# Kernel tuning notes

Hardware: AMD Instinct MI355X
Metric: run time of the kernel (lower is better)

Reference implementation:

```python
import jax, jax.numpy as jnp
import numpy as np

ALPHA = 1.702   # GLU sigmoid scale
LIMIT = 7.0     # clamp limit
K = 2           # experts per token


def setup_inputs() -> dict:
    key = jax.random.key(0)
    ks = jax.random.split(key, 4)
    B, S, H, E, I = 1, 1024, 1024, 8, 1024
    return {
        "hidden_states": jax.random.normal(ks[0], (B, S, H), jnp.float32),
        "router_weight": jax.random.normal(ks[1], (E, H), jnp.float32),
        "router_bias": jnp.zeros((E,), jnp.float32),
        "gate_up_proj": jax.random.normal(ks[2], (E, H, 2 * I), jnp.float32) * 0.02,
        "gate_up_bias": jnp.zeros((E, 2 * I), jnp.float32),
        "down_proj": jax.random.normal(ks[3], (E, I, H), jnp.float32) * 0.02,
        "down_bias": jnp.zeros((E, H), jnp.float32),
    }


def reference(hidden_states, router_weight, router_bias, gate_up_proj,
              gate_up_bias, down_proj, down_bias):
    B, S, H = hidden_states.shape
    E = router_weight.shape[0]
    I = down_proj.shape[1]
    T = B * S

    flat = hidden_states.reshape(T, H)

    # Router: softmax over experts, top-K selection (weights NOT renormalized).
    logits = flat @ router_weight.T + router_bias               # [T, E]
    scores = jax.nn.softmax(logits, axis=-1)
    topk_vals, topk_idx = jax.lax.top_k(scores, K)              # [T, K]

    # Dense per-token expert weight matrix (equivalent of dispatch metadata +
    # combine * topk_weights in the tt pipeline); top-k indices are unique.
    w = jnp.zeros((T, E), scores.dtype).at[
        jnp.arange(T)[:, None], topk_idx].set(topk_vals)        # [T, E]

    # Expert MLP with clamped GLU (gpt-oss style).
    gu = jnp.einsum('th,ehf->tef', flat, gate_up_proj) + gate_up_bias  # [T,E,2I]
    gate = jnp.minimum(gu[..., :I], LIMIT)
    up = jnp.clip(gu[..., I:], -LIMIT, LIMIT)
    glu = gate * jax.nn.sigmoid(gate * ALPHA)
    act = (up + 1.0) * glu                                       # [T, E, I]

    down = jnp.einsum('tei,eih->teh', act, down_proj) + down_bias  # [T, E, H]

    # Weighted combine over selected experts.
    out = jnp.einsum('teh,te->th', down, w)
    return out.reshape(B, S, H)
```

## Files before the change

### kernel.cpp

```cpp
#include <hip/hip_runtime.h>
#include <hip/hip_bf16.h>


typedef unsigned short u16;
typedef __attribute__((ext_vector_type(8))) __bf16 bf16x8;
typedef __attribute__((ext_vector_type(4))) float f32x4;

#define T_TOK 1024
#define H_DIM 1024
#define E_NUM 8
#define I_DIM 1024
#define ALPHA 1.702f
#define LIMIT 7.0f
#define LSTR 72

__device__ __forceinline__ u16 f2bf(float f) {
    unsigned u = __builtin_bit_cast(unsigned, f);
    u = (u + 0x7FFFu + ((u >> 16) & 1u)) >> 16;
    return (u16)u;
}

__device__ __forceinline__ unsigned pk2(float lo, float hi) {
#if defined(__has_builtin) && __has_builtin(__builtin_amdgcn_cvt_pk_bf16_f32)
    typedef __attribute__((ext_vector_type(2))) __bf16 bf16x2_t;
    bf16x2_t v = __builtin_amdgcn_cvt_pk_bf16_f32(lo, hi);
    return __builtin_bit_cast(unsigned, v);
#else
    return (unsigned)f2bf(lo) | ((unsigned)f2bf(hi) << 16);
#endif
}

__device__ __forceinline__ f32x4 mfma16(bf16x8 a, bf16x8 b, f32x4 c) {
    return __builtin_amdgcn_mfma_f32_16x16x32_bf16(a, b, c, 0, 0, 0);
}

__device__ __forceinline__ void expert_range(const int* counts, int e,
                                             int& cnt, int& abase) {
    int a = 0, c = 0;
#pragma unroll
    for (int i = 0; i < E_NUM; ++i) {
        int v = counts[i];
        if (i < e) a += v;
        if (i == e) c = v;
    }
    cnt = c; abase = a;
}

__global__ void k_zero(int* counts) {
    if (threadIdx.x < E_NUM) counts[threadIdx.x] = 0;
}

__global__ __launch_bounds__(256) void k_router(
    const float* __restrict__ x, const float* __restrict__ rw,
    const float* __restrict__ rb, const float* __restrict__ db,
    int* __restrict__ counts, int* __restrict__ tok_list,
    float* __restrict__ w_list, u16* __restrict__ xb,
    float* __restrict__ out)
{
    const int t = blockIdx.x;
    const int tid = threadIdx.x;
    const float4 xv = *(const float4*)(x + (size_t)t * H_DIM + tid * 4);

    *(uint2*)(xb + (size_t)t * H_DIM + tid * 4) =
        make_uint2(pk2(xv.x, xv.y), pk2(xv.z, xv.w));

    float p[E_NUM];
#pragma unroll
    for (int e = 0; e < E_NUM; ++e) {
        const float4 wv = *(const float4*)(rw + e * H_DIM + tid * 4);
        p[e] = xv.x * wv.x + xv.y * wv.y + xv.z * wv.z + xv.w * wv.w;
    }
#pragma unroll
    for (int off = 32; off; off >>= 1) {
#pragma unroll
        for (int e = 0; e < E_NUM; ++e) p[e] += __shfl_down(p[e], off, 64);
    }
    __shared__ float red[4][E_NUM];
    __shared__ int se[2];
    __shared__ float sw[2];
    const int lane = tid & 63, wvid = tid >> 6;
    if (lane == 0) {
#pragma unroll
        for (int e = 0; e < E_NUM; ++e) red[wvid][e] = p[e];
    }
    __syncthreads();
    if (tid == 0) {
        float lg[E_NUM];
#pragma unroll
        for (int e = 0; e < E_NUM; ++e)
            lg[e] = red[0][e] + red[1][e] + red[2][e] + red[3][e] + rb[e];
        float m1 = -1e30f, m2 = -1e30f; int i1 = 0, i2 = 0;
#pragma unroll
        for (int e = 0; e < E_NUM; ++e) {
            float l = lg[e];
            if (l > m1) { m2 = m1; i2 = i1; m1 = l; i1 = e; }
            else if (l > m2) { m2 = l; i2 = e; }
        }
        float s = 0.f;
#pragma unroll
        for (int e = 0; e < E_NUM; ++e) s += __expf(lg[e] - m1);
        const float w0 = 1.0f / s;
        const float w1 = __expf(m2 - m1) / s;
        int slot0 = atomicAdd(&counts[i1], 1);
        tok_list[i1 * T_TOK + slot0] = t;
        w_list[i1 * T_TOK + slot0] = w0;
        int slot1 = atomicAdd(&counts[i2], 1);
        tok_list[i2 * T_TOK + slot1] = t;
        w_list[i2 * T_TOK + slot1] = w1;
        se[0] = i1; se[1] = i2; sw[0] = w0; sw[1] = w1;
    }
    __syncthreads();
    const int e0 = se[0], e1 = se[1];
    const float w0 = sw[0], w1 = sw[1];
    const int c = tid * 4;
    float4 d0 = *(const float4*)(db + e0 * H_DIM + c);
    float4 d1 = *(const float4*)(db + e1 * H_DIM + c);
    float4 o;
    o.x = w0 * d0.x + w1 * d1.x;
    o.y = w0 * d0.y + w1 * d1.y;
    o.z = w0 * d0.z + w1 * d1.z;
    o.w = w0 * d0.w + w1 * d1.w;
    *(float4*)(out + (size_t)t * H_DIM + c) = o;
}

__global__ __launch_bounds__(256, 4) void k_gateup(
    const float* __restrict__ gup, const float* __restrict__ gub,
    const int* __restrict__ counts, const int* __restrict__ tok_list,
    const u16* __restrict__ xb, u16* __restrict__ act)
{
    const int e = blockIdx.z;
    int cnt, abase;
    expert_range(counts, e, cnt, abase);
    const int m0 = blockIdx.y * 64;
    if (m0 >= cnt) return;
    const int n0 = blockIdx.x * 32;
    const int tid = threadIdx.x;

    __shared__ __align__(16) u16 As0[64 * LSTR];
    __shared__ __align__(16) u16 Bs0[64 * LSTR];
    __shared__ __align__(16) u16 As1[64 * LSTR];
    __shared__ __align__(16) u16 Bs1[64 * LSTR];
    unsigned* B32_0 = (unsigned*)Bs0;
    unsigned* B32_1 = (unsigned*)Bs1;

    const int arow_i = tid >> 2, akq = (tid & 3) * 16;
    const int aslot = m0 + arow_i;
    const int atok = (aslot < cnt) ? tok_list[e * T_TOK + aslot] : 0;
    const u16* asrc = xb + (size_t)atok * H_DIM + akq;
    u16* adst0 = &As0[arow_i * LSTR + akq];
    u16* adst1 = &As1[arow_i * LSTR + akq];

    const int kp = tid >> 3, q = tid & 7;
    const float* bgate = gup + ((size_t)e << 21) + n0 + q * 4;

    const int lane = tid & 63, wv = tid >> 6;
    const int fm = lane & 15, kg = lane >> 4;

    f32x4 accg[2], accu[2];
#pragma unroll
    for (int nt = 0; nt < 2; ++nt) {
        accg[nt] = (f32x4){0.f, 0.f, 0.f, 0.f};
        accu[nt] = (f32x4){0.f, 0.f, 0.f, 0.f};
    }

#define GU_LOAD(A0, A1, G0, G1, U0, U1, KB)                                    \
    {                                                                          \
        const u16* ap_ = asrc + (KB);                                          \
        A0 = *(const uint4*)(ap_);                                             \
        A1 = *(const uint4*)(ap_ + 8);                                         \
        const float* gp_ = bgate + (size_t)((KB) + 2 * kp) * 2048;             \
        G0 = *(const float4*)(gp_);                                            \
        G1 = *(const float4*)(gp_ + 2048);                                     \
        U0 = *(const float4*)(gp_ + 1024);                                     \
        U1 = *(const float4*)(gp_ + 3072);                                     \
    }
#define GU_STORE(AD, B32, A0, A1, G0, G1, U0, U1)                              \
    {                                                                          \
        *(uint4*)(AD)       = A0;                                              \
        *(uint4*)((AD) + 8) = A1;                                              \
        const float* g0_ = (const float*)&G0; const float* g1_ = (const float*)&G1; \
        const float* u0_ = (const float*)&U0; const float* u1_ = (const float*)&U1; \
        _Pragma("unroll")                                                      \
        for (int j = 0; j < 4; ++j) {                                          \
            B32[(q * 4 + j) * 36 + kp]        = pk2(g0_[j], g1_[j]);           \
            B32[(32 + q * 4 + j) * 36 + kp]   = pk2(u0_[j], u1_[j]);           \
        }                                                                      \
    }
#define GU_MFMA(AS, BS)                                                        \
    {                                                                          \
        _Pragma("unroll")                                                      \
        for (int sub = 0; sub < 2; ++sub) {                                    \
            bf16x8 af = *(const bf16x8*)&AS[(wv * 16 + fm) * LSTR + sub * 32 + kg * 8]; \
            _Pragma("unroll")                                                  \
            for (int nt = 0; nt < 2; ++nt) {                                   \
                bf16x8 bg = *(const bf16x8*)&BS[(nt * 16 + fm) * LSTR + sub * 32 + kg * 8]; \
                bf16x8 bu = *(const bf16x8*)&BS[(32 + nt * 16 + fm) * LSTR + sub * 32 + kg * 8]; \
                accg[nt] = mfma16(af, bg, accg[nt]);                           \
                accu[nt] = mfma16(af, bu, accu[nt]);                           \
            }                                                                  \
        }                                                                      \
    }

    uint4 a0s0, a1s0, a0s1, a1s1;
    float4 g0s0, g1s0, u0s0, u1s0, g0s1, g1s1, u0s1, u1s1;
    GU_LOAD(a0s0, a1s0, g0s0, g1s0, u0s0, u1s0, 0);
    GU_LOAD(a0s1, a1s1, g0s1, g1s1, u0s1, u1s1, 64);
    GU_STORE(adst0, B32_0, a0s0, a1s0, g0s0, g1s0, u0s0, u1s0);
    GU_LOAD(a0s0, a1s0, g0s0, g1s0, u0s0, u1s0, 128);
    __syncthreads();

    for (int kb = 0; kb < H_DIM; kb += 128) {
        GU_STORE(adst1, B32_1, a0s1, a1s1, g0s1, g1s1, u0s1, u1s1);
        if (kb + 192 < H_DIM)
            GU_LOAD(a0s1, a1s1, g0s1, g1s1, u0s1, u1s1, kb + 192);
        GU_MFMA(As0, Bs0);
        __syncthreads();
        if (kb + 128 < H_DIM) {
            GU_STORE(adst0, B32_0, a0s0, a1s0, g0s0, g1s0, u0s0, u1s0);
            if (kb + 256 < H_DIM)
                GU_LOAD(a0s0, a1s0, g0s0, g1s0, u0s0, u1s0, kb + 256);
        }
        GU_MFMA(As1, Bs1);
        __syncthreads();
    }
#undef GU_LOAD
#undef GU_STORE
#undef GU_MFMA

#pragma unroll
    for (int r = 0; r < 4; ++r) {
        int rowb = wv * 16 + kg * 4 + r;
        int slot = m0 + rowb;
        if (slot >= cnt) continue;
        size_t arow_o = (size_t)(abase + slot) * I_DIM;
#pragma unroll
        for (int nt = 0; nt < 2; ++nt) {
            int cn = n0 + nt * 16 + fm;
            float g = accg[nt][r] + gub[e * 2048 + cn];
            float u = accu[nt][r] + gub[e * 2048 + 1024 + cn];
            g = fminf(g, LIMIT);
            u = fminf(fmaxf(u, -LIMIT), LIMIT);
            float glu = g / (1.f + __expf(-ALPHA * g));
            act[arow_o + cn] = f2bf((u + 1.f) * glu);
        }
    }
}

__global__ __launch_bounds__(256, 4) void k_down(
    const float* __restrict__ dp,
    const int* __restrict__ counts, const int* __restrict__ tok_list,
    const float* __restrict__ w_list,
    const u16* __restrict__ act, float* __restrict__ out)
{
    const int e = blockIdx.z & 7, ks = blockIdx.z >> 3;
    int cnt, abase;
    expert_range(counts, e, cnt, abase);
    const int m0 = blockIdx.y * 64;
    if (m0 >= cnt) return;
    const int n0 = blockIdx.x * 64;
    const int tid = threadIdx.x;

    __shared__ __align__(16) u16 As0[64 * LSTR];
    __shared__ __align__(16) u16 Bs0[64 * LSTR];
    __shared__ __align__(16) u16 As1[64 * LSTR];
    __shared__ __align__(16) u16 Bs1[64 * LSTR];
    unsigned* B32_0 = (unsigned*)Bs0;
    unsigned* B32_1 = (unsigned*)Bs1;

    const int arow_i = tid >> 2, akq = (tid & 3) * 16;
    const u16* asrc = act + (size_t)(abase + m0 + arow_i) * I_DIM + ks * 512 + akq;
    u16* adst0 = &As0[arow_i * LSTR + akq];
    u16* adst1 = &As1[arow_i * LSTR + akq];

    const int kp = tid >> 3, q = tid & 7;
    const float* bsrc = dp + ((size_t)e << 20) + (size_t)(ks * 512) * 1024 + n0 + q * 4;

    const int lane = tid & 63, wv = tid >> 6;
    const int fm = lane & 15, kg = lane >> 4;

    f32x4 acc[4];
#pragma unroll
    for (int nt = 0; nt < 4; ++nt) acc[nt] = (f32x4){0.f, 0.f, 0.f, 0.f};

#define DN_LOAD(A0, A1, B00, B01, B10, B11, KB)                                \
    {                                                                          \
        const u16* ap_ = asrc + (KB);                                          \
        A0 = *(const uint4*)(ap_);                                             \
        A1 = *(const uint4*)(ap_ + 8);                                         \
        const float* bp_ = bsrc + (size_t)((KB) + 2 * kp) * 1024;              \
        B00 = *(const float4*)(bp_);                                           \
        B01 = *(const float4*)(bp_ + 1024);                                    \
        B10 = *(const float4*)(bp_ + 32);                                      \
        B11 = *(const float4*)(bp_ + 1056);                                    \
    }
#define DN_STORE(AD, B32, A0, A1, B00, B01, B10, B11)                          \
    {                                                                          \
        *(uint4*)(AD)       = A0;                                              \
        *(uint4*)((AD) + 8) = A1;                                              \
        const float* b00_ = (const float*)&B00; const float* b01_ = (const float*)&B01; \
        const float* b10_ = (const float*)&B10; const float* b11_ = (const float*)&B11; \
        _Pragma("unroll")                                                      \
        for (int j = 0; j < 4; ++j) {                                          \
            B32[(q * 4 + j) * 36 + kp]      = pk2(b00_[j], b01_[j]);           \
            B32[(32 + q * 4 + j) * 36 + kp] = pk2(b10_[j], b11_[j]);           \
        }                                                                      \
    }
#define DN_MFMA(AS, BS)                                                        \
    {                                                                          \
        _Pragma("unroll")                                                      \
        for (int sub = 0; sub < 2; ++sub) {                                    \
            bf16x8 af = *(const bf16x8*)&AS[(wv * 16 + fm) * LSTR + sub * 32 + kg * 8]; \
            _Pragma("unroll")                                                  \
            for (int nt = 0; nt < 4; ++nt) {                                   \
                bf16x8 b = *(const bf16x8*)&BS[(nt * 16 + fm) * LSTR + sub * 32 + kg * 8]; \
                acc[nt] = mfma16(af, b, acc[nt]);                              \
            }                                                                  \
        }                                                                      \
    }

    uint4 a0s0, a1s0, a0s1, a1s1;
    float4 b00s0, b01s0, b10s0, b11s0, b00s1, b01s1, b10s1, b11s1;
    DN_LOAD(a0s0, a1s0, b00s0, b01s0, b10s0, b11s0, 0);
    DN_LOAD(a0s1, a1s1, b00s1, b01s1, b10s1, b11s1, 64);
    DN_STORE(adst0, B32_0, a0s0, a1s0, b00s0, b01s0, b10s0, b11s0);
    DN_LOAD(a0s0, a1s0, b00s0, b01s0, b10s0, b11s0, 128);
    __syncthreads();

    for (int kb = 0; kb < 512; kb += 128) {
        DN_STORE(adst1, B32_1, a0s1, a1s1, b00s1, b01s1, b10s1, b11s1);
        if (kb + 192 < 512)
            DN_LOAD(a0s1, a1s1, b00s1, b01s1, b10s1, b11s1, kb + 192);
        DN_MFMA(As0, Bs0);
        __syncthreads();
        if (kb + 128 < 512) {
            DN_STORE(adst0, B32_0, a0s0, a1s0, b00s0, b01s0, b10s0, b11s0);
            if (kb + 256 < 512)
                DN_LOAD(a0s0, a1s0, b00s0, b01s0, b10s0, b11s0, kb + 256);
        }
        DN_MFMA(As1, Bs1);
        __syncthreads();
    }
#undef DN_LOAD
#undef DN_STORE
#undef DN_MFMA

#pragma unroll
    for (int r = 0; r < 4; ++r) {
        int rowb = wv * 16 + kg * 4 + r;
        int slot = m0 + rowb;
        if (slot >= cnt) continue;
        float wgt = w_list[e * T_TOK + slot];
        int tok = tok_list[e * T_TOK + slot];
        float* orow = out + (size_t)tok * H_DIM + n0;
#pragma unroll
        for (int nt = 0; nt < 4; ++nt)
            atomicAdd(orow + nt * 16 + fm, acc[nt][r] * wgt);
    }
}

extern "C" void kernel_launch(void* const* d_in, const int* in_sizes, int n_in,
                              void* d_out, int out_size, void* d_ws, size_t ws_size,
                              hipStream_t stream) {
    const float* x   = (const float*)d_in[0];
    const float* rw  = (const float*)d_in[1];
    const float* rb  = (const float*)d_in[2];
    const float* gup = (const float*)d_in[3];
    const float* gub = (const float*)d_in[4];
    const float* dp  = (const float*)d_in[5];
    const float* db  = (const float*)d_in[6];
    float* out = (float*)d_out;

    char* ws = (char*)d_ws;
    int*   counts   = (int*)(ws);
    int*   tok_list = (int*)(ws + 64);
    float* w_list   = (float*)(ws + 64 + 32768);
    u16*   xb       = (u16*)(ws + 65600);
    u16*   act      = (u16*)(ws + 65600 + 2097152);

    k_zero<<<1, 64, 0, stream>>>(counts);
    k_router<<<T_TOK, 256, 0, stream>>>(x, rw, rb, db, counts, tok_list, w_list,
                                        xb, out);
    k_gateup<<<dim3(32, 16, 8), 256, 0, stream>>>(gup, gub, counts, tok_list,
                                                  xb, act);
    k_down<<<dim3(16, 16, 16), 256, 0, stream>>>(dp, counts, tok_list, w_list,
                                                 act, out);
}
```

Baseline: 213.8 us.

## Pre-convert expert weights to transposed bf16 and stage tiles via global_load_lds

Adds a conversion kernel that turns gate_up and down weights into transposed bf16 buffers in workspace on every call. The GEMM kernels then load A and B tiles straight into LDS with global_load_lds, replacing register staging and per-element packing. The MFMA tiling changes to a 2x2 wave layout. The aim is to cut global bandwidth in the GEMMs and drop the in-loop fp32-to-bf16 packing. The cost is an extra full pass over all expert weights each call, plus unpadded LDS rows that may cause bank conflicts.

Result: slower. 221.0 us (+3.4%).

```diff
diff --git a/kernel.cpp b/kernel.cpp
--- a/kernel.cpp
+++ b/kernel.cpp
@@ -12,7 +12,6 @@
 #define I_DIM 1024
 #define ALPHA 1.702f
 #define LIMIT 7.0f
-#define LSTR 72
 
 __device__ __forceinline__ u16 f2bf(float f) {
     unsigned u = __builtin_bit_cast(unsigned, f);
@@ -34,6 +33,12 @@
     return __builtin_amdgcn_mfma_f32_16x16x32_bf16(a, b, c, 0, 0, 0);
 }
 
+__device__ __forceinline__ void gld16(const void* g, void* l) {
+    __builtin_amdgcn_global_load_lds(
+        (const __attribute__((address_space(1))) void*)g,
+        (__attribute__((address_space(3))) void*)l, 16, 0, 0);
+}
+
 __device__ __forceinline__ void expert_range(const int* counts, int e,
                                              int& cnt, int& abase) {
     int a = 0, c = 0;
@@ -46,8 +51,40 @@
     cnt = c; abase = a;
 }
 
-__global__ void k_zero(int* counts) {
-    if (threadIdx.x < E_NUM) counts[threadIdx.x] = 0;
+__global__ __launch_bounds__(256) void k_cvt(
+    const float* __restrict__ gup, const float* __restrict__ dp,
+    u16* __restrict__ gupT, u16* __restrict__ dpT, int* __restrict__ counts)
+{
+    if (blockIdx.x == 0 && threadIdx.x < E_NUM) counts[threadIdx.x] = 0;
+    const int b = blockIdx.x;
+    const float* src; u16* dst; int C, k0, c0;
+    if (b < 4096) {
+        int e = b >> 9, t = b & 511;
+        k0 = (t >> 5) * 64; c0 = (t & 31) * 64;
+        src = gup + ((size_t)e << 21); dst = gupT + ((size_t)e << 21); C = 2048;
+    } else {
+        int b2 = b - 4096;
+        int e = b2 >> 8, t = b2 & 255;
+        k0 = (t >> 4) * 64; c0 = (t & 15) * 64;
+        src = dp + ((size_t)e << 20); dst = dpT + ((size_t)e << 20); C = 1024;
+    }
+    __shared__ u16 Ls[64][72];
+    const int tid = threadIdx.x;
+    const int rr = tid >> 4, cc = (tid & 15) * 4;
+#pragma unroll
+    for (int i = 0; i < 4; ++i) {
+        int k = rr + i * 16;
+        float4 v = *(const float4*)(src + (size_t)(k0 + k) * C + c0 + cc);
+        Ls[cc + 0][k] = f2bf(v.x);
+        Ls[cc + 1][k] = f2bf(v.y);
+        Ls[cc + 2][k] = f2bf(v.z);
+        Ls[cc + 3][k] = f2bf(v.w);
+    }
+    __syncthreads();
+    const int oc = tid >> 2, och = (tid & 3) * 16;
+    u16* orow = dst + (size_t)(c0 + oc) * 1024 + k0 + och;
+    *(uint4*)(orow)     = *(uint4*)&Ls[oc][och];
+    *(uint4*)(orow + 8) = *(uint4*)&Ls[oc][och + 8];
 }
 
 __global__ __launch_bounds__(256) void k_router(
@@ -124,7 +161,7 @@
 }
 
 __global__ __launch_bounds__(256, 4) void k_gateup(
-    const float* __restrict__ gup, const float* __restrict__ gub,
+    const u16* __restrict__ gupT, const float* __restrict__ gub,
     const int* __restrict__ counts, const int* __restrict__ tok_list,
     const u16* __restrict__ xb, u16* __restrict__ act)
 {
@@ -135,119 +172,94 @@
     if (m0 >= cnt) return;
     const int n0 = blockIdx.x * 32;
     const int tid = threadIdx.x;
-
-    __shared__ __align__(16) u16 As0[64 * LSTR];
-    __shared__ __align__(16) u16 Bs0[64 * LSTR];
-    __shared__ __align__(16) u16 As1[64 * LSTR];
-    __shared__ __align__(16) u16 Bs1[64 * LSTR];
-    unsigned* B32_0 = (unsigned*)Bs0;
-    unsigned* B32_1 = (unsigned*)Bs1;
-
-    const int arow_i = tid >> 2, akq = (tid & 3) * 16;
-    const int aslot = m0 + arow_i;
-    const int atok = (aslot < cnt) ? tok_list[e * T_TOK + aslot] : 0;
-    const u16* asrc = xb + (size_t)atok * H_DIM + akq;
-    u16* adst0 = &As0[arow_i * LSTR + akq];
-    u16* adst1 = &As1[arow_i * LSTR + akq];
-
-    const int kp = tid >> 3, q = tid & 7;
-    const float* bgate = gup + ((size_t)e << 21) + n0 + q * 4;
-
     const int lane = tid & 63, wv = tid >> 6;
     const int fm = lane & 15, kg = lane >> 4;
+    const int wm = wv >> 1, wn = wv & 1;
+
+    __shared__ __align__(16) u16 As0[64 * 64], As1[64 * 64];
+    __shared__ __align__(16) u16 Bs0[64 * 64], Bs1[64 * 64];
+
+    const int lr = lane >> 3, lk = (lane & 7) * 8;
+    const u16* gA[2];
+#pragma unroll
+    for (int i = 0; i < 2; ++i) {
+        int row = (wv * 2 + i) * 8 + lr;
+        int slot = m0 + row;
+        int tok = (slot < cnt) ? tok_list[e * T_TOK + slot] : 0;
+        gA[i] = xb + (size_t)tok * H_DIM + lk;
+    }
+    const u16* gB[2];
+#pragma unroll
+    for (int i = 0; i < 2; ++i) {
+        int row = (wv * 2 + i) * 8 + lr;
+        int col = (row < 32) ? (n0 + row) : (1024 + n0 + row - 32);
+        gB[i] = gupT + ((size_t)e << 21) + (size_t)col * 1024 + lk;
+    }
 
     f32x4 accg[2], accu[2];
 #pragma unroll
-    for (int nt = 0; nt < 2; ++nt) {
-        accg[nt] = (f32x4){0.f, 0.f, 0.f, 0.f};
-        accu[nt] = (f32x4){0.f, 0.f, 0.f, 0.f};
-    }
-
-#define GU_LOAD(A0, A1, G0, G1, U0, U1, KB)                                    \
+    for (int m = 0; m < 2; ++m) {
+        accg[m] = (f32x4){0.f, 0.f, 0.f, 0.f};
+        accu[m] = (f32x4){0.f, 0.f, 0.f, 0.f};
+    }
+
+#define GU_STAGE(AS, BS, KB)                                                   \
     {                                                                          \
-        const u16* ap_ = asrc + (KB);                                          \
-        A0 = *(const uint4*)(ap_);                                             \
-        A1 = *(const uint4*)(ap_ + 8);                                         \
-        const float* gp_ = bgate + (size_t)((KB) + 2 * kp) * 2048;             \
-        G0 = *(const float4*)(gp_);                                            \
-        G1 = *(const float4*)(gp_ + 2048);                                     \
-        U0 = *(const float4*)(gp_ + 1024);                                     \
-        U1 = *(const float4*)(gp_ + 3072);                                     \
-    }
-#define GU_STORE(AD, B32, A0, A1, G0, G1, U0, U1)                              \
-    {                                                                          \
-        *(uint4*)(AD)       = A0;                                              \
-        *(uint4*)((AD) + 8) = A1;                                              \
-        const float* g0_ = (const float*)&G0; const float* g1_ = (const float*)&G1; \
-        const float* u0_ = (const float*)&U0; const float* u1_ = (const float*)&U1; \
-        _Pragma("unroll")                                                      \
-        for (int j = 0; j < 4; ++j) {                                          \
-            B32[(q * 4 + j) * 36 + kp]        = pk2(g0_[j], g1_[j]);           \
-            B32[(32 + q * 4 + j) * 36 + kp]   = pk2(u0_[j], u1_[j]);           \
-        }                                                                      \
+        gld16(gA[0] + (KB), (u16*)(AS) + (wv * 2 + 0) * 512);                  \
+        gld16(gA[1] + (KB), (u16*)(AS) + (wv * 2 + 1) * 512);                  \
+        gld16(gB[0] + (KB), (u16*)(BS) + (wv * 2 + 0) * 512);                  \
+        gld16(gB[1] + (KB), (u16*)(BS) + (wv * 2 + 1) * 512);                  \
     }
 #define GU_MFMA(AS, BS)                                                        \
     {                                                                          \
         _Pragma("unroll")                                                      \
-        for (int sub = 0; sub < 2; ++sub) {                                    \
-            bf16x8 af = *(const bf16x8*)&AS[(wv * 16 + fm) * LSTR + sub * 32 + kg * 8]; \
-            _Pragma("unroll")                                                  \
-            for (int nt = 0; nt < 2; ++nt) {                                   \
-                bf16x8 bg = *(const bf16x8*)&BS[(nt * 16 + fm) * LSTR + sub * 32 + kg * 8]; \
-                bf16x8 bu = *(const bf16x8*)&BS[(32 + nt * 16 + fm) * LSTR + sub * 32 + kg * 8]; \
-                accg[nt] = mfma16(af, bg, accg[nt]);                           \
-                accu[nt] = mfma16(af, bu, accu[nt]);                           \
-            }                                                                  \
+        for (int ks = 0; ks < 2; ++ks) {                                       \
+            const int ko = ks * 32 + kg * 8;                                   \
+            bf16x8 a0 = *(const bf16x8*)((const u16*)(AS) + (wm * 32 + fm) * 64 + ko);      \
+            bf16x8 a1 = *(const bf16x8*)((const u16*)(AS) + (wm * 32 + 16 + fm) * 64 + ko); \
+            bf16x8 bg = *(const bf16x8*)((const u16*)(BS) + (wn * 16 + fm) * 64 + ko);      \
+            bf16x8 bu = *(const bf16x8*)((const u16*)(BS) + (32 + wn * 16 + fm) * 64 + ko); \
+            accg[0] = mfma16(a0, bg, accg[0]);                                 \
+            accu[0] = mfma16(a0, bu, accu[0]);                                 \
+            accg[1] = mfma16(a1, bg, accg[1]);                                 \
+            accu[1] = mfma16(a1, bu, accu[1]);                                 \
         }                                                                      \
     }
 
-    uint4 a0s0, a1s0, a0s1, a1s1;
-    float4 g0s0, g1s0, u0s0, u1s0, g0s1, g1s1, u0s1, u1s1;
-    GU_LOAD(a0s0, a1s0, g0s0, g1s0, u0s0, u1s0, 0);
-    GU_LOAD(a0s1, a1s1, g0s1, g1s1, u0s1, u1s1, 64);
-    GU_STORE(adst0, B32_0, a0s0, a1s0, g0s0, g1s0, u0s0, u1s0);
-    GU_LOAD(a0s0, a1s0, g0s0, g1s0, u0s0, u1s0, 128);
-    __syncthreads();
-
+    GU_STAGE(As0, Bs0, 0);
+    __syncthreads();
     for (int kb = 0; kb < H_DIM; kb += 128) {
-        GU_STORE(adst1, B32_1, a0s1, a1s1, g0s1, g1s1, u0s1, u1s1);
-        if (kb + 192 < H_DIM)
-            GU_LOAD(a0s1, a1s1, g0s1, g1s1, u0s1, u1s1, kb + 192);
+        GU_STAGE(As1, Bs1, kb + 64);
         GU_MFMA(As0, Bs0);
         __syncthreads();
-        if (kb + 128 < H_DIM) {
-            GU_STORE(adst0, B32_0, a0s0, a1s0, g0s0, g1s0, u0s0, u1s0);
-            if (kb + 256 < H_DIM)
-                GU_LOAD(a0s0, a1s0, g0s0, g1s0, u0s0, u1s0, kb + 256);
-        }
+        if (kb + 128 < H_DIM) GU_STAGE(As0, Bs0, kb + 128);
         GU_MFMA(As1, Bs1);
         __syncthreads();
     }
-#undef GU_LOAD
-#undef GU_STORE
+#undef GU_STAGE
 #undef GU_MFMA
 
 #pragma unroll
-    for (int r = 0; r < 4; ++r) {
-        int rowb = wv * 16 + kg * 4 + r;
-        int slot = m0 + rowb;
-        if (slot >= cnt) continue;
-        size_t arow_o = (size_t)(abase + slot) * I_DIM;
-#pragma unroll
-        for (int nt = 0; nt < 2; ++nt) {
-            int cn = n0 + nt * 16 + fm;
-            float g = accg[nt][r] + gub[e * 2048 + cn];
-            float u = accu[nt][r] + gub[e * 2048 + 1024 + cn];
+    for (int m = 0; m < 2; ++m) {
+#pragma unroll
+        for (int r = 0; r < 4; ++r) {
+            int row = wm * 32 + m * 16 + kg * 4 + r;
+            int slot = m0 + row;
+            if (slot >= cnt) continue;
+            size_t arow = (size_t)(abase + slot) * I_DIM;
+            int cn = n0 + wn * 16 + fm;
+            float g = accg[m][r] + gub[e * 2048 + cn];
+            float u = accu[m][r] + gub[e * 2048 + 1024 + cn];
             g = fminf(g, LIMIT);
             u = fminf(fmaxf(u, -LIMIT), LIMIT);
             float glu = g / (1.f + __expf(-ALPHA * g));
-            act[arow_o + cn] = f2bf((u + 1.f) * glu);
+            act[arow + cn] = f2bf((u + 1.f) * glu);
         }
     }
 }
 
 __global__ __launch_bounds__(256, 4) void k_down(
-    const float* __restrict__ dp,
+    const u16* __restrict__ dpT,
     const int* __restrict__ counts, const int* __restrict__ tok_list,
     const float* __restrict__ w_list,
     const u16* __restrict__ act, float* __restrict__ out)
@@ -259,102 +271,81 @@
     if (m0 >= cnt) return;
     const int n0 = blockIdx.x * 64;
     const int tid = threadIdx.x;
-
-    __shared__ __align__(16) u16 As0[64 * LSTR];
-    __shared__ __align__(16) u16 Bs0[64 * LSTR];
-    __shared__ __align__(16) u16 As1[64 * LSTR];
-    __shared__ __align__(16) u16 Bs1[64 * LSTR];
-    unsigned* B32_0 = (unsigned*)Bs0;
-    unsigned* B32_1 = (unsigned*)Bs1;
-
-    const int arow_i = tid >> 2, akq = (tid & 3) * 16;
-    const u16* asrc = act + (size_t)(abase + m0 + arow_i) * I_DIM + ks * 512 + akq;
-    u16* adst0 = &As0[arow_i * LSTR + akq];
-    u16* adst1 = &As1[arow_i * LSTR + akq];
-
-    const int kp = tid >> 3, q = tid & 7;
-    const float* bsrc = dp + ((size_t)e << 20) + (size_t)(ks * 512) * 1024 + n0 + q * 4;
-
     const int lane = tid & 63, wv = tid >> 6;
     const int fm = lane & 15, kg = lane >> 4;
-
-    f32x4 acc[4];
-#pragma unroll
-    for (int nt = 0; nt < 4; ++nt) acc[nt] = (f32x4){0.f, 0.f, 0.f, 0.f};
-
-#define DN_LOAD(A0, A1, B00, B01, B10, B11, KB)                                \
+    const int wm = wv >> 1, wn = wv & 1;
+
+    __shared__ __align__(16) u16 As0[64 * 64], As1[64 * 64];
+    __shared__ __align__(16) u16 Bs0[64 * 64], Bs1[64 * 64];
+
+    const int lr = lane >> 3, lk = (lane & 7) * 8;
+    const u16* gA[2];
+    const u16* gB[2];
+#pragma unroll
+    for (int i = 0; i < 2; ++i) {
+        int row = (wv * 2 + i) * 8 + lr;
+        gA[i] = act + (size_t)(abase + m0 + row) * I_DIM + ks * 512 + lk;
+        gB[i] = dpT + ((size_t)e << 20) + (size_t)(n0 + row) * 1024 + ks * 512 + lk;
+    }
+
+    f32x4 acc[2][2];
+#pragma unroll
+    for (int m = 0; m < 2; ++m)
+#pragma unroll
+        for (int n = 0; n < 2; ++n) acc[m][n] = (f32x4){0.f, 0.f, 0.f, 0.f};
+
+#define DN_STAGE(AS, BS, KB)                                                   \
     {                                                                          \
-        const u16* ap_ = asrc + (KB);                                          \
-        A0 = *(const uint4*)(ap_);                                             \
-        A1 = *(const uint4*)(ap_ + 8);                                         \
-        const float* bp_ = bsrc + (size_t)((KB) + 2 * kp) * 1024;              \
-        B00 = *(const float4*)(bp_);                                           \
-        B01 = *(const float4*)(bp_ + 1024);                                    \
-        B10 = *(const float4*)(bp_ + 32);                                      \
-        B11 = *(const float4*)(bp_ + 1056);                                    \
-    }
-#define DN_STORE(AD, B32, A0, A1, B00, B01, B10, B11)                          \
-    {                                                                          \
-        *(uint4*)(AD)       = A0;                                              \
-        *(uint4*)((AD) + 8) = A1;                                              \
-        const float* b00_ = (const float*)&B00; const float* b01_ = (const float*)&B01; \
-        const float* b10_ = (const float*)&B10; const float* b11_ = (const float*)&B11; \
-        _Pragma("unroll")                                                      \
-        for (int j = 0; j < 4; ++j) {                                          \
-            B32[(q * 4 + j) * 36 + kp]      = pk2(b00_[j], b01_[j]);           \
-            B32[(32 + q * 4 + j) * 36 + kp] = pk2(b10_[j], b11_[j]);           \
-        }                                                                      \
+        gld16(gA[0] + (KB), (u16*)(AS) + (wv * 2 + 0) * 512);                  \
+        gld16(gA[1] + (KB), (u16*)(AS) + (wv * 2 + 1) * 512);                  \
+        gld16(gB[0] + (KB), (u16*)(BS) + (wv * 2 + 0) * 512);                  \
+        gld16(gB[1] + (KB), (u16*)(BS) + (wv * 2 + 1) * 512);                  \
     }
 #define DN_MFMA(AS, BS)                                                        \
     {                                                                          \
         _Pragma("unroll")                                                      \
-        for (int sub = 0; sub < 2; ++sub) {                                    \
-            bf16x8 af = *(const bf16x8*)&AS[(wv * 16 + fm) * LSTR + sub * 32 + kg * 8]; \
-            _Pragma("unroll")                                                  \
-            for (int nt = 0; nt < 4; ++nt) {                                   \
-                bf16x8 b = *(const bf16x8*)&BS[(nt * 16 + fm) * LSTR + sub * 32 + kg * 8]; \
-                acc[nt] = mfma16(af, b, acc[nt]);                              \
-            }                                                                  \
+        for (int ks2 = 0; ks2 < 2; ++ks2) {                                    \
+            const int ko = ks2 * 32 + kg * 8;                                  \
+            bf16x8 a0 = *(const bf16x8*)((const u16*)(AS) + (wm * 32 + fm) * 64 + ko);      \
+            bf16x8 a1 = *(const bf16x8*)((const u16*)(AS) + (wm * 32 + 16 + fm) * 64 + ko); \
+            bf16x8 b0 = *(const bf16x8*)((const u16*)(BS) + (wn * 32 + fm) * 64 + ko);      \
+            bf16x8 b1 = *(const bf16x8*)((const u16*)(BS) + (wn * 32 + 16 + fm) * 64 + ko); \
+            acc[0][0] = mfma16(a0, b0, acc[0][0]);                             \
+            acc[0][1] = mfma16(a0, b1, acc[0][1]);                             \
+            acc[1][0] = mfma16(a1, b0, acc[1][0]);                             \
+            acc[1][1] = mfma16(a1, b1, acc[1][1]);                             \
         }                                                                      \
     }
 
-    uint4 a0s0, a1s0, a0s1, a1s1;
-    float4 b00s0, b01s0, b10s0, b11s0, b00s1, b01s1, b10s1, b11s1;
-    DN_LOAD(a0s0, a1s0, b00s0, b01s0, b10s0, b11s0, 0);
-    DN_LOAD(a0s1, a1s1, b00s1, b01s1, b10s1, b11s1, 64);
-    DN_STORE(adst0, B32_0, a0s0, a1s0, b00s0, b01s0, b10s0, b11s0);
-    DN_LOAD(a0s0, a1s0, b00s0, b01s0, b10s0, b11s0, 128);
-    __syncthreads();
-
+    DN_STAGE(As0, Bs0, 0);
+    __syncthreads();
     for (int kb = 0; kb < 512; kb += 128) {
-        DN_STORE(adst1, B32_1, a0s1, a1s1, b00s1, b01s1, b10s1, b11s1);
-        if (kb + 192 < 512)
-            DN_LOAD(a0s1, a1s1, b00s1, b01s1, b10s1, b11s1, kb + 192);
+        DN_STAGE(As1, Bs1, kb + 64);
         DN_MFMA(As0, Bs0);
         __syncthreads();
-        if (kb + 128 < 512) {
-            DN_STORE(adst0, B32_0, a0s0, a1s0, b00s0, b01s0, b10s0, b11s0);
-            if (kb + 256 < 512)
-                DN_LOAD(a0s0, a1s0, b00s0, b01s0, b10s0, b11s0, kb + 256);
-        }
+        if (kb + 128 < 512) DN_STAGE(As0, Bs0, kb + 128);
         DN_MFMA(As1, Bs1);
         __syncthreads();
     }
-#undef DN_LOAD
-#undef DN_STORE
+#undef DN_STAGE
 #undef DN_MFMA
 
 #pragma unroll
-    for (int r = 0; r < 4; ++r) {
-        int rowb = wv * 16 + kg * 4 + r;
-        int slot = m0 + rowb;
-        if (slot >= cnt) continue;
-        float wgt = w_list[e * T_TOK + slot];
-        int tok = tok_list[e * T_TOK + slot];
-        float* orow = out + (size_t)tok * H_DIM + n0;
-#pragma unroll
-        for (int nt = 0; nt < 4; ++nt)
-            atomicAdd(orow + nt * 16 + fm, acc[nt][r] * wgt);
+    for (int m = 0; m < 2; ++m) {
+#pragma unroll
+        for (int r = 0; r < 4; ++r) {
+            int row = wm * 32 + m * 16 + kg * 4 + r;
+            int slot = m0 + row;
+            if (slot >= cnt) continue;
+            float wgt = w_list[e * T_TOK + slot];
+            int tok = tok_list[e * T_TOK + slot];
+            float* orow = out + (size_t)tok * H_DIM;
+#pragma unroll
+            for (int n = 0; n < 2; ++n) {
+                int col = n0 + wn * 32 + n * 16 + fm;
+                atomicAdd(orow + col, acc[m][n][r] * wgt);
+            }
+        }
     }
 }
 
@@ -376,12 +367,14 @@
     float* w_list   = (float*)(ws + 64 + 32768);
     u16*   xb       = (u16*)(ws + 65600);
     u16*   act      = (u16*)(ws + 65600 + 2097152);
-
-    k_zero<<<1, 64, 0, stream>>>(counts);
+    u16*   gupT     = (u16*)(ws + 8388608);
+    u16*   dpT      = (u16*)(ws + 41943040);
+
+    k_cvt<<<6144, 256, 0, stream>>>(gup, dp, gupT, dpT, counts);
     k_router<<<T_TOK, 256, 0, stream>>>(x, rw, rb, db, counts, tok_list, w_list,
                                         xb, out);
-    k_gateup<<<dim3(32, 16, 8), 256, 0, stream>>>(gup, gub, counts, tok_list,
+    k_gateup<<<dim3(32, 16, 8), 256, 0, stream>>>(gupT, gub, counts, tok_list,
                                                   xb, act);
-    k_down<<<dim3(16, 16, 16), 256, 0, stream>>>(dp, counts, tok_list, w_list,
+    k_down<<<dim3(16, 16, 16), 256, 0, stream>>>(dpT, counts, tok_list, w_list,
                                                  act, out);
 }
```
